# Kernel tuning notes

Hardware: AMD Instinct MI355X
Metric: run time of the kernel (lower is better)

## Reference

```python
import jax, jax.numpy as jnp
import numpy as np

N = 80000
E = 1280000
EPS = 1e-5

def _lrelu(x):
    return jax.nn.leaky_relu(x, 0.01)

def _bn(h):
    # training-mode BatchNorm1d with batch size 1: stats over the node dim; affine is identity at init
    return (h - h.mean(0)) / jnp.sqrt(h.var(0) + EPS)

def _ln(h, g, b):
    m = h.mean(-1, keepdims=True)
    v = h.var(-1, keepdims=True)
    return (h - m) / jnp.sqrt(v + EPS) * g + b

def _gcn(h, w, b, src, dst, n):
    # PyG GCNConv: add self loops, symmetric deg^-1/2 normalization, aggregate at target
    hw = h @ w.T
    loop = jnp.arange(n, dtype=src.dtype)
    s = jnp.concatenate([src, loop])
    d = jnp.concatenate([dst, loop])
    deg = jax.ops.segment_sum(jnp.ones(d.shape, hw.dtype), d, num_segments=n)
    dinv = jnp.where(deg > 0, 1.0 / jnp.sqrt(deg), 0.0)
    msg = hw[s] * (dinv[s] * dinv[d])[:, None]  # [E+N, C]
    return jax.ops.segment_sum(msg, d, num_segments=n) + b

def _tnet(x, c1w, c1b, c2w, c2b, c3w, c3b, f1w, f1b, f2w, f2b, f3w, f3b):
    h = jax.nn.relu(x @ c1w.T + c1b)          # [N,64]  (source skips bn1)
    h = jax.nn.relu(_bn(h @ c2w.T + c2b))     # [N,128]
    h = jax.nn.relu(_bn(h @ c3w.T + c3b))     # [N,1024]
    g = h.max(0)                              # global max pool -> [1024]
    g = jax.nn.relu(g @ f1w.T + f1b)
    g = jax.nn.relu(g @ f2w.T + f2b)
    iden = jnp.array([1.0, 0.0, 0.0, 0.0, 1.0, 0.0, 0.0, 0.0, 1.0], x.dtype)
    g = g @ f3w.T + f3b + iden
    return g.reshape(3, 3)

def _forward(edge_index, x, tnet_c1_w, tnet_c1_b, tnet_c2_w, tnet_c2_b, tnet_c3_w, tnet_c3_b, tnet_fc1_w, tnet_fc1_b, tnet_fc2_w, tnet_fc2_b, tnet_fc3_w, tnet_fc3_b, conv1_w, conv1_b, g1_li_w, g1_li_b, g1_gcn_w, g1_gcn_b, g1_ln_g, g1_ln_b, conv2_w, conv2_b, g2_li_w, g2_li_b, g2_gcn_w, g2_gcn_b, g2_ln_g, g2_ln_b, conv3_w, conv3_b, out_w, out_b):
    src, dst = edge_index[0], edge_index[1]
    n = x.shape[0]
    T = _tnet(x, tnet_c1_w, tnet_c1_b, tnet_c2_w, tnet_c2_b, tnet_c3_w, tnet_c3_b, tnet_fc1_w, tnet_fc1_b, tnet_fc2_w, tnet_fc2_b, tnet_fc3_w, tnet_fc3_b)
    h0 = x @ T                                  # [N,3] spatial transform
    xg = _lrelu(h0 @ conv1_w.T + conv1_b)       # [N,64] (conv1d k=1 == per-node linear)
    # Gcn_Attention 1
    nf = _lrelu(xg @ g1_li_w.T + g1_li_b)
    nf2 = _lrelu(_gcn(nf, g1_gcn_w, g1_gcn_b, src, dst, n))
    h = _ln(jnp.concatenate([nf, nf2], 1), g1_ln_g, g1_ln_b)   # [N,128]
    h = _lrelu(h @ conv2_w.T + conv2_b)
    # Gcn_Attention 2
    nf = _lrelu(h @ g2_li_w.T + g2_li_b)
    nf2 = _lrelu(_gcn(nf, g2_gcn_w, g2_gcn_b, src, dst, n))
    h = _ln(jnp.concatenate([nf, nf2], 1), g2_ln_g, g2_ln_b)   # [N,256]
    h = jnp.concatenate([h, xg], 1)                            # [N,320]
    h = _lrelu(h @ conv3_w.T + conv3_b)                        # [N,256]
    pooled = h.mean(0)                                         # global mean pool (single graph)
    feat = jnp.concatenate([jnp.broadcast_to(pooled, (n, pooled.shape[0])), xg], 1)  # [N,320]
    return feat @ out_w.T + out_b                              # [N,4]

def setup_inputs():
    ki = iter(jax.random.split(jax.random.key(0), 32))
    def W(shape):
        return jax.random.normal(next(ki), shape, jnp.float32) * (1.0 / float(np.sqrt(shape[-1])))
    z = lambda n: jnp.zeros((n,), jnp.float32)
    o = lambda n: jnp.ones((n,), jnp.float32)
    inp = {}
    inp['x'] = jax.random.normal(next(ki), (N, 3), jnp.float32)
    inp['edge_index'] = jax.random.randint(next(ki), (2, E), 0, N, dtype=jnp.int32)
    inp['tnet_c1_w'] = W((64, 3)); inp['tnet_c1_b'] = z(64)
    inp['tnet_c2_w'] = W((128, 64)); inp['tnet_c2_b'] = z(128)
    inp['tnet_c3_w'] = W((1024, 128)); inp['tnet_c3_b'] = z(1024)
    inp['tnet_fc1_w'] = W((512, 1024)); inp['tnet_fc1_b'] = z(512)
    inp['tnet_fc2_w'] = W((256, 512)); inp['tnet_fc2_b'] = z(256)
    inp['tnet_fc3_w'] = W((9, 256)); inp['tnet_fc3_b'] = z(9)
    inp['conv1_w'] = W((64, 3)); inp['conv1_b'] = z(64)
    inp['g1_li_w'] = W((64, 64)); inp['g1_li_b'] = z(64)
    inp['g1_gcn_w'] = W((64, 64)); inp['g1_gcn_b'] = z(64)
    inp['g1_ln_g'] = o(128); inp['g1_ln_b'] = z(128)
    inp['conv2_w'] = W((128, 128)); inp['conv2_b'] = z(128)
    inp['g2_li_w'] = W((128, 128)); inp['g2_li_b'] = z(128)
    inp['g2_gcn_w'] = W((128, 128)); inp['g2_gcn_b'] = z(128)
    inp['g2_ln_g'] = o(256); inp['g2_ln_b'] = z(256)
    inp['conv3_w'] = W((256, 320)); inp['conv3_b'] = z(256)
    inp['out_w'] = W((4, 320)); inp['out_b'] = z(4)
    return inp

def reference(x, edge_index, tnet_c1_w, tnet_c1_b, tnet_c2_w, tnet_c2_b, tnet_c3_w, tnet_c3_b, tnet_fc1_w, tnet_fc1_b, tnet_fc2_w, tnet_fc2_b, tnet_fc3_w, tnet_fc3_b, conv1_w, conv1_b, g1_li_w, g1_li_b, g1_gcn_w, g1_gcn_b, g1_ln_g, g1_ln_b, conv2_w, conv2_b, g2_li_w, g2_li_b, g2_gcn_w, g2_gcn_b, g2_ln_g, g2_ln_b, conv3_w, conv3_b, out_w, out_b):
    return _forward(edge_index, x, tnet_c1_w, tnet_c1_b, tnet_c2_w, tnet_c2_b, tnet_c3_w, tnet_c3_b, tnet_fc1_w, tnet_fc1_b, tnet_fc2_w, tnet_fc2_b, tnet_fc3_w, tnet_fc3_b, conv1_w, conv1_b, g1_li_w, g1_li_b, g1_gcn_w, g1_gcn_b, g1_ln_g, g1_ln_b, conv2_w, conv2_b, g2_li_w, g2_li_b, g2_gcn_w, g2_gcn_b, g2_ln_g, g2_ln_b, conv3_w, conv3_b, out_w, out_b)
```

## Files before the change

### kernel.cpp

```cpp
#include <hip/hip_runtime.h>
#include <cstddef>

#define EPSV 1e-5f

typedef __attribute__((ext_vector_type(8))) short frag8;
typedef __attribute__((ext_vector_type(4))) float f32x4;

__device__ __forceinline__ float lrelu01(float v) { return v > 0.f ? v : 0.01f * v; }
__device__ __forceinline__ void atomAddF(float* p, float v) { unsafeAtomicAdd(p, v); }
__device__ __forceinline__ unsigned fkey(float f) {
    unsigned u = __float_as_uint(f);
    return (u & 0x80000000u) ? ~u : (u | 0x80000000u);
}
__device__ __forceinline__ unsigned short f2b(float f) {
    unsigned u = __float_as_uint(f);
    unsigned r = u + 0x7fffu + ((u >> 16) & 1u);
    return (unsigned short)(r >> 16);
}
__device__ __forceinline__ float b2f(unsigned short h) {
    return __uint_as_float(((unsigned)h) << 16);
}
__device__ __forceinline__ float blo(unsigned u) { return __uint_as_float(u << 16); }
__device__ __forceinline__ float bhi(unsigned u) { return __uint_as_float(u & 0xffff0000u); }

static inline unsigned cdivu(unsigned a, unsigned b) { return (a + b - 1) / b; }


__global__ void k_degrank(const int* __restrict__ dst, int* __restrict__ deg,
                          int* __restrict__ rank, int E) {
    int e = blockIdx.x * 256 + threadIdx.x;
    if (e < E) rank[e] = atomicAdd(&deg[dst[e]], 1);
}

__global__ void k_scan_local(const int* __restrict__ deg, int* __restrict__ startv,
                             int* __restrict__ bsum, float* __restrict__ dinv, int n) {
    __shared__ int t0[256];
    int tid = threadIdx.x;
    int i = blockIdx.x * 256 + tid;
    int v = (i < n) ? deg[i] : 0;
    if (i < n) dinv[i] = rsqrtf((float)(v + 1));
    t0[tid] = v;
    __syncthreads();
    for (int o = 1; o < 256; o <<= 1) {
        int add = (tid >= o) ? t0[tid - o] : 0;
        __syncthreads();
        t0[tid] += add;
        __syncthreads();
    }
    if (i < n) startv[i] = t0[tid] - v;
    if (tid == 255) bsum[blockIdx.x] = t0[255];
}

__global__ void k_scan_bsum(int* __restrict__ bsum, int nb) {
    __shared__ int t0[512];
    int tid = threadIdx.x;
    int v = (tid < nb) ? bsum[tid] : 0;
    t0[tid] = v;
    __syncthreads();
    for (int o = 1; o < 512; o <<= 1) {
        int add = (tid >= o) ? t0[tid - o] : 0;
        __syncthreads();
        t0[tid] += add;
        __syncthreads();
    }
    if (tid < nb) bsum[tid] = t0[tid] - v;
}

__global__ void k_scan_add(int* __restrict__ startv, const int* __restrict__ bsum, int n) {
    int i = blockIdx.x * 256 + threadIdx.x;
    if (i < n) startv[i] += bsum[blockIdx.x];
}

__global__ void k_fill(const int* __restrict__ src, const int* __restrict__ dst,
                       const int* __restrict__ rank, const int* __restrict__ startv,
                       int* __restrict__ csr, int E) {
    int e = blockIdx.x * 256 + threadIdx.x;
    if (e < E) csr[startv[dst[e]] + rank[e]] = src[e];
}

template <int CH>
__launch_bounds__(256)
__global__ void k_gln(const int* __restrict__ startv, const int* __restrict__ degv,
                      const int* __restrict__ csr, const unsigned short* __restrict__ q,
                      const unsigned short* __restrict__ nf, const float* __restrict__ dinv,
                      const float* __restrict__ gcn_b, const float* __restrict__ lng,
                      const float* __restrict__ lnb, unsigned short* __restrict__ outp,
                      int ldo, int n) {
    const int wv = threadIdx.x >> 6, lane = threadIdx.x & 63;
    const int g = lane >> 4, p = lane & 15;
    int node = blockIdx.x * 4 + wv;
    if (node >= n) return;
    constexpr int CPL = CH / 16;
    constexpr int DPL = CPL / 2;

    float acc[CPL];
#pragma unroll
    for (int k = 0; k < CPL; ++k) acc[k] = 0.f;

    {
        unsigned su[DPL];
        const unsigned short* qrow = q + (size_t)node * CH + p * CPL;
        if (DPL == 4) *(uint4*)su = *(const uint4*)qrow;
        else          *(uint2*)su = *(const uint2*)qrow;
        if (g == 0) {
#pragma unroll
            for (int d = 0; d < DPL; ++d) { acc[2 * d] += blo(su[d]); acc[2 * d + 1] += bhi(su[d]); }
        }
    }

    int s0 = startv[node], cnt = degv[node];
    int sidx[4];
#pragma unroll
    for (int t = 0; t < 4; ++t) { int j = t * 4 + g; sidx[t] = (j < cnt) ? csr[s0 + j] : 0; }
    for (int j0 = 0; j0 < cnt; j0 += 16) {
        unsigned buf[4][DPL];
#pragma unroll
        for (int t = 0; t < 4; ++t) {
            const unsigned short* src = q + (size_t)sidx[t] * CH + p * CPL;
            if (DPL == 4) *(uint4*)buf[t] = *(const uint4*)src;
            else          *(uint2*)buf[t] = *(const uint2*)src;
        }
        int nsidx[4];
#pragma unroll
        for (int t = 0; t < 4; ++t) {
            int j = j0 + 16 + t * 4 + g;
            nsidx[t] = (j < cnt) ? csr[s0 + j] : 0;
        }
#pragma unroll
        for (int t = 0; t < 4; ++t) {
            if (j0 + t * 4 + g < cnt) {
#pragma unroll
                for (int d = 0; d < DPL; ++d) {
                    acc[2 * d] += blo(buf[t][d]);
                    acc[2 * d + 1] += bhi(buf[t][d]);
                }
            }
        }
#pragma unroll
        for (int t = 0; t < 4; ++t) sidx[t] = nsidx[t];
    }

#pragma unroll
    for (int k = 0; k < CPL; ++k) {
        acc[k] += __shfl_xor(acc[k], 16);
        acc[k] += __shfl_xor(acc[k], 32);
    }

    float di = dinv[node];
    float nv[CPL], bv[CPL];
    {
        unsigned su[DPL];
        const unsigned short* nrow = nf + (size_t)node * CH + p * CPL;
        if (DPL == 4) *(uint4*)su = *(const uint4*)nrow;
        else          *(uint2*)su = *(const uint2*)nrow;
#pragma unroll
        for (int d = 0; d < DPL; ++d) { nv[2 * d] = blo(su[d]); nv[2 * d + 1] = bhi(su[d]); }
    }
    const float* gb = gcn_b + p * CPL;
#pragma unroll
    for (int k = 0; k < CPL; ++k) bv[k] = lrelu01(di * acc[k] + gb[k]);

    float s = 0.f, ss = 0.f;
#pragma unroll
    for (int k = 0; k < CPL; ++k) { s += nv[k] + bv[k]; ss += nv[k] * nv[k] + bv[k] * bv[k]; }
#pragma unroll
    for (int off = 32; off > 0; off >>= 1) { s += __shfl_xor(s, off); ss += __shfl_xor(ss, off); }
    const float inv = 1.f / (float)(8 * CH);
    float mu = s * inv;
    float var = ss * inv - mu * mu;
    float rsg = rsqrtf(var + EPSV);

    unsigned short* orow = outp + (size_t)node * ldo;
    if (g == 0) {
        unsigned short tmp[CPL];
        const float* lg = lng + p * CPL; const float* lb = lnb + p * CPL;
#pragma unroll
        for (int k = 0; k < CPL; ++k) tmp[k] = f2b((nv[k] - mu) * rsg * lg[k] + lb[k]);
        if (DPL == 4) *(uint4*)(orow + p * CPL) = *(uint4*)tmp;
        else          *(uint2*)(orow + p * CPL) = *(uint2*)tmp;
    } else if (g == 1) {
        unsigned short tmp[CPL];
        const float* lg = lng + CH + p * CPL; const float* lb = lnb + CH + p * CPL;
#pragma unroll
        for (int k = 0; k < CPL; ++k) tmp[k] = f2b((bv[k] - mu) * rsg * lg[k] + lb[k]);
        if (DPL == 4) *(uint4*)(orow + CH + p * CPL) = *(uint4*)tmp;
        else          *(uint2*)(orow + CH + p * CPL) = *(uint2*)tmp;
    }
}


__global__ void k_wconv(const float* __restrict__ s0, const float* __restrict__ s1,
                        const float* __restrict__ s2, const float* __restrict__ s3,
                        const float* __restrict__ s4, const float* __restrict__ s5,
                        const float* __restrict__ s6, const float* __restrict__ s7,
                        unsigned short* __restrict__ dst) {
    int t = blockIdx.x * 256 + threadIdx.x;
    if (t >= 278528) return;
    const float* srcs[8] = {s0, s1, s2, s3, s4, s5, s6, s7};
    const int off[9] = {0, 8192, 139264, 143360, 147456, 163840, 180224, 196608, 278528};
    int seg = 0;
    while (t >= off[seg + 1]) ++seg;
    unsigned short v = f2b(srcs[seg][t - off[seg]]);
    if (seg == 1) {
        int li = t - 8192;
        int rch = li >> 7, k = li & 127;
        int cb = rch >> 7, r = rch & 127;
        int flat = ((r >> 4) * 4 + (k >> 5)) * 64 + ((k >> 3) & 3) * 16 + (r & 15);
        dst[8192 + cb * 16384 + flat * 8 + (k & 7)] = v;
    } else {
        dst[t] = v;
    }
}

__global__ void k_h1(const float* __restrict__ x, const float* __restrict__ w,
                     const float* __restrict__ b, unsigned short* __restrict__ h1, int n) {
    int node = blockIdx.x * 256 + threadIdx.x;
    if (node >= n) return;
    float x0 = x[node * 3], x1 = x[node * 3 + 1], x2 = x[node * 3 + 2];
    unsigned short* o = h1 + (size_t)node * 64;
#pragma unroll
    for (int cp = 0; cp < 8; ++cp) {
        unsigned short tmp[8];
#pragma unroll
        for (int t = 0; t < 8; ++t) {
            int c = cp * 8 + t;
            float v = x0 * w[c * 3] + x1 * w[c * 3 + 1] + x2 * w[c * 3 + 2] + b[c];
            tmp[t] = f2b(fmaxf(v, 0.f));
        }
        *(float4*)(o + cp * 8) = *(float4*)tmp;
    }
}

__global__ void k_prebn(const float* __restrict__ z, const float* __restrict__ sum2,
                        const float* __restrict__ ss2, unsigned short* __restrict__ a3f,
                        int n16, float invn) {
    int t = blockIdx.x * 256 + threadIdx.x;
    if (t >= n16) return;
    int row = t >> 4, cp = t & 15;
    int c = cp * 8;
    const float* src = z + (size_t)row * 128 + c;
    float4 v0 = *(const float4*)src;
    float4 v1 = *(const float4*)(src + 4);
    float vv[8] = {v0.x, v0.y, v0.z, v0.w, v1.x, v1.y, v1.z, v1.w};
    unsigned short o[8];
#pragma unroll
    for (int i = 0; i < 8; ++i) {
        float m = sum2[c + i] * invn;
        float var = ss2[c + i] * invn - m * m;
        o[i] = f2b(fmaxf((vv[i] - m) * rsqrtf(var + EPSV), 0.f));
    }
    int tile = row >> 7, r = row & 127;
    int flat = ((r >> 4) * 4 + (cp >> 2)) * 64 + (cp & 3) * 16 + (r & 15);
    *(float4*)(a3f + (size_t)tile * 16384 + flat * 8) = *(float4*)o;
}

__launch_bounds__(256)
__global__ void k_fc1(const float* __restrict__ sum3, const float* __restrict__ ss3,
                      const unsigned* __restrict__ maxk,
                      const float* __restrict__ f1w, const float* __restrict__ f1b,
                      float* __restrict__ a1, float invn) {
    __shared__ float g[1024];
    int tid = threadIdx.x;
    for (int c = tid; c < 1024; c += 256) {
        float m = sum3[c] * invn;
        float var = ss3[c] * invn - m * m;
        unsigned k = maxk[c];
        unsigned u = (k & 0x80000000u) ? (k & 0x7FFFFFFFu) : ~k;
        g[c] = fmaxf((__uint_as_float(u) - m) * rsqrtf(var + EPSV), 0.f);
    }
    __syncthreads();
    int row = blockIdx.x * 64 + (tid >> 2);
    int part = tid & 3;
    const float* w = f1w + (size_t)row * 1024 + part * 256;
    const float* gg = g + part * 256;
    float s = 0.f;
    for (int k = 0; k < 256; ++k) s = fmaf(w[k], gg[k], s);
    s += __shfl_xor(s, 1); s += __shfl_xor(s, 2);
    if (part == 0) a1[row] = fmaxf(s + f1b[row], 0.f);
}

__launch_bounds__(256)
__global__ void k_fc23(const float* __restrict__ a1, const float* __restrict__ f2w,
                       const float* __restrict__ f2b, const float* __restrict__ f3w,
                       const float* __restrict__ f3b, float* __restrict__ T9) {
    __shared__ float a2[256];
    int tid = threadIdx.x;
    {
        const float* w = f2w + (size_t)tid * 512;
        float s = f2b[tid];
        for (int k = 0; k < 512; ++k) s = fmaf(w[k], a1[k], s);
        a2[tid] = fmaxf(s, 0.f);
    }
    __syncthreads();
    if (tid < 9) {
        const float* w = f3w + (size_t)tid * 256;
        float s = f3b[tid];
        for (int k = 0; k < 256; ++k) s = fmaf(w[k], a2[k], s);
        if (tid == 0 || tid == 4 || tid == 8) s += 1.f;
        T9[tid] = s;
    }
}

__global__ void k_xg(const float* __restrict__ x, const float* __restrict__ T9,
                     const float* __restrict__ w, const float* __restrict__ b,
                     unsigned short* __restrict__ xg, int n) {
    int node = blockIdx.x * 256 + threadIdx.x;
    if (node >= n) return;
    float x0 = x[node * 3], x1 = x[node * 3 + 1], x2 = x[node * 3 + 2];
    float h0 = x0 * T9[0] + x1 * T9[3] + x2 * T9[6];
    float h1 = x0 * T9[1] + x1 * T9[4] + x2 * T9[7];
    float h2 = x0 * T9[2] + x1 * T9[5] + x2 * T9[8];
    unsigned short* o = xg + (size_t)node * 320;
#pragma unroll
    for (int cp = 0; cp < 8; ++cp) {
        unsigned short tmp[8];
#pragma unroll
        for (int t = 0; t < 8; ++t) {
            int c = cp * 8 + t;
            float v = h0 * w[c * 3] + h1 * w[c * 3 + 1] + h2 * w[c * 3 + 2] + b[c];
            tmp[t] = f2b(lrelu01(v));
        }
        *(float4*)(o + cp * 8) = *(float4*)tmp;
    }
}

__global__ void k_const4(const float* __restrict__ pooled, const float* __restrict__ ow,
                         const float* __restrict__ ob, float* __restrict__ c4, float invn) {
    int j = threadIdx.x >> 6, lane = threadIdx.x & 63;
    float s = 0.f;
    for (int c = lane; c < 256; c += 64) s += pooled[c] * invn * ow[j * 320 + c];
#pragma unroll
    for (int off = 32; off > 0; off >>= 1) s += __shfl_down(s, off);
    if (lane == 0) c4[j] = s + ob[j];
}

__global__ void k_out(const unsigned short* __restrict__ hcat, const float* __restrict__ ow,
                      const float* __restrict__ c4, float* __restrict__ out, int n) {
    int node = blockIdx.x * 256 + threadIdx.x;
    if (node >= n) return;
    const unsigned short* xgp = hcat + (size_t)node * 320 + 256;
    float s0 = c4[0], s1 = c4[1], s2 = c4[2], s3 = c4[3];
#pragma unroll
    for (int cp = 0; cp < 8; ++cp) {
        float4 raw = *(const float4*)(xgp + cp * 8);
        unsigned short tmp[8];
        *(float4*)tmp = raw;
#pragma unroll
        for (int t = 0; t < 8; ++t) {
            int k = 256 + cp * 8 + t;
            float f = b2f(tmp[t]);
            s0 = fmaf(f, ow[k], s0);
            s1 = fmaf(f, ow[320 + k], s1);
            s2 = fmaf(f, ow[640 + k], s2);
            s3 = fmaf(f, ow[960 + k], s3);
        }
    }
    *(float4*)(out + (size_t)node * 4) = make_float4(s0, s1, s2, s3);
}

enum { MF_BIAS = 1, MF_LRELU = 2, MF_DINV = 4, MF_STOREF = 8, MF_STOREB = 16,
       MF_STATS = 32, MF_COLSUM = 64 };

template <int BN, int MODE>
__launch_bounds__(256)
__global__ void k_mgemm(const unsigned short* __restrict__ A, int lda, int K,
                        const unsigned short* __restrict__ W,
                        const float* __restrict__ bias,
                        float* __restrict__ OutF, unsigned short* __restrict__ OutB, int ldo,
                        const float* __restrict__ dinv,
                        float* __restrict__ sum_o, float* __restrict__ ss_o,
                        unsigned* __restrict__ maxk_o) {
    constexpr int BM = 128;
    constexpr int LDT = 40;
    __shared__ unsigned short As[BM * LDT];
    __shared__ unsigned short Ws[BN * LDT];
    __shared__ float redS[2 * 128];
    __shared__ unsigned redM[128];

    const int tid = threadIdx.x;
    const int wid = tid >> 6, lane = tid & 63;
    const int quad = lane >> 4, lrow = lane & 15;
    const int bn0 = blockIdx.x * BM;
    const int bc0 = blockIdx.y * BN;

    constexpr int NI = (BN == 128) ? 4 : 2;
    constexpr int NJ = 4;
    const int wm = (BN == 128) ? (wid & 1) * 64 : wid * 32;
    const int wn = (BN == 128) ? (wid >> 1) * 64 : 0;

    if (MODE & (MF_STATS | MF_COLSUM)) {
        for (int c = tid; c < BN; c += 256) {
            redS[c] = 0.f; redS[128 + c] = 0.f; redM[c] = 0u;
        }
    }

    f32x4 acc[NI][NJ] = {};

    for (int k0 = 0; k0 < K; k0 += 32) {
#pragma unroll
        for (int h = 0; h < 2; ++h) {
            int ch = tid + h * 256;
            int row = ch >> 2, cp = ch & 3;
            const unsigned short* src = A + (size_t)(bn0 + row) * lda + k0 + cp * 8;
            *(float4*)&As[row * LDT + cp * 8] = *(const float4*)src;
        }
#pragma unroll
        for (int h = 0; h < BN / 64; ++h) {
            int ch = tid + h * 256;
            int row = ch >> 2, cp = ch & 3;
            const unsigned short* src = W + (size_t)(bc0 + row) * K + k0 + cp * 8;
            *(float4*)&Ws[row * LDT + cp * 8] = *(const float4*)src;
        }
        __syncthreads();
        frag8 af[NI], bf[NJ];
#pragma unroll
        for (int i = 0; i < NI; ++i)
            af[i] = *(const frag8*)&As[(wm + i * 16 + lrow) * LDT + quad * 8];
#pragma unroll
        for (int j = 0; j < NJ; ++j)
            bf[j] = *(const frag8*)&Ws[(wn + j * 16 + lrow) * LDT + quad * 8];
#pragma unroll
        for (int i = 0; i < NI; ++i)
#pragma unroll
            for (int j = 0; j < NJ; ++j)
                acc[i][j] = __builtin_amdgcn_mfma_f32_16x16x32_bf16(af[i], bf[j], acc[i][j], 0, 0, 0);
        __syncthreads();
    }

#pragma unroll
    for (int j = 0; j < NJ; ++j) {
        const int col = bc0 + wn + j * 16 + lrow;
        float bv = (MODE & MF_BIAS) ? bias[col] : 0.f;
        float s = 0.f, q = 0.f, m = -3.4e38f;
#pragma unroll
        for (int i = 0; i < NI; ++i) {
            const int rowb = bn0 + wm + i * 16 + quad * 4;
#pragma unroll
            for (int r = 0; r < 4; ++r) {
                float t = acc[i][j][r] + bv;
                if (MODE & MF_LRELU) t = lrelu01(t);
                if (MODE & MF_DINV) t *= dinv[rowb + r];
                if (MODE & MF_STOREF) OutF[(size_t)(rowb + r) * ldo + col] = t;
                if (MODE & MF_STOREB) OutB[(size_t)(rowb + r) * ldo + col] = f2b(t);
                s += t; q += t * t; m = fmaxf(m, t);
            }
        }
        if (MODE & (MF_STATS | MF_COLSUM)) {
            s += __shfl_xor(s, 16); s += __shfl_xor(s, 32);
            if (MODE & MF_STATS) {
                q += __shfl_xor(q, 16); q += __shfl_xor(q, 32);
                m = fmaxf(m, __shfl_xor(m, 16)); m = fmaxf(m, __shfl_xor(m, 32));
            }
            if (quad == 0) {
                int lc = wn + j * 16 + lrow;
                atomicAdd(&redS[lc], s);
                if (MODE & MF_STATS) {
                    atomicAdd(&redS[128 + lc], q);
                    atomicMax(&redM[lc], fkey(m));
                }
            }
        }
    }
    if (MODE & (MF_STATS | MF_COLSUM)) {
        __syncthreads();
        for (int c = tid; c < BN; c += 256) {
            atomAddF(&sum_o[bc0 + c], redS[c]);
            if (MODE & MF_STATS) {
                atomAddF(&ss_o[bc0 + c], redS[128 + c]);
                atomicMax(&maxk_o[bc0 + c], redM[c]);
            }
        }
    }
}

template <int BN>
__launch_bounds__(256)
__global__ void k_ligc(const unsigned short* __restrict__ A, int lda, int K,
                       const unsigned short* __restrict__ Wli, const float* __restrict__ bli,
                       const unsigned short* __restrict__ Wgc, const float* __restrict__ dinv,
                       unsigned short* __restrict__ NF, int ldnf,
                       unsigned short* __restrict__ Q, int ldq) {
    constexpr int BM = 128;
    constexpr int LDT = 40;
    constexpr int LDT2 = BN + 8;
    __shared__ unsigned short SA[BM * LDT2];
    __shared__ unsigned short Ws[BN * LDT];

    const int tid = threadIdx.x;
    const int wid = tid >> 6, lane = tid & 63;
    const int quad = lane >> 4, lrow = lane & 15;
    const int bn0 = blockIdx.x * BM;
    constexpr int NI = (BN == 128) ? 4 : 2;
    constexpr int NJ = 4;
    const int wm = (BN == 128) ? (wid & 1) * 64 : wid * 32;
    const int wn = (BN == 128) ? (wid >> 1) * 64 : 0;

    {
        f32x4 acc[NI][NJ] = {};
        for (int k0 = 0; k0 < K; k0 += 32) {
#pragma unroll
            for (int h = 0; h < 2; ++h) {
                int ch = tid + h * 256;
                int row = ch >> 2, cp = ch & 3;
                *(float4*)&SA[row * LDT + cp * 8] =
                    *(const float4*)(A + (size_t)(bn0 + row) * lda + k0 + cp * 8);
            }
#pragma unroll
            for (int h = 0; h < BN / 64; ++h) {
                int ch = tid + h * 256;
                int row = ch >> 2, cp = ch & 3;
                *(float4*)&Ws[row * LDT + cp * 8] =
                    *(const float4*)(Wli + (size_t)row * K + k0 + cp * 8);
            }
            __syncthreads();
            frag8 af[NI], bf[NJ];
#pragma unroll
            for (int i = 0; i < NI; ++i)
                af[i] = *(const frag8*)&SA[(wm + i * 16 + lrow) * LDT + quad * 8];
#pragma unroll
            for (int j = 0; j < NJ; ++j)
                bf[j] = *(const frag8*)&Ws[(wn + j * 16 + lrow) * LDT + quad * 8];
#pragma unroll
            for (int i = 0; i < NI; ++i)
#pragma unroll
                for (int j = 0; j < NJ; ++j)
                    acc[i][j] = __builtin_amdgcn_mfma_f32_16x16x32_bf16(af[i], bf[j], acc[i][j], 0, 0, 0);
            __syncthreads();
        }
#pragma unroll
        for (int j = 0; j < NJ; ++j) {
            const int col = wn + j * 16 + lrow;
            float bv = bli[col];
#pragma unroll
            for (int i = 0; i < NI; ++i) {
                const int rowl = wm + i * 16 + quad * 4;
#pragma unroll
                for (int r = 0; r < 4; ++r) {
                    unsigned short h = f2b(lrelu01(acc[i][j][r] + bv));
                    NF[(size_t)(bn0 + rowl + r) * ldnf + col] = h;
                    SA[(rowl + r) * LDT2 + col] = h;
                }
            }
        }
        __syncthreads();
    }
    {
        f32x4 acc[NI][NJ] = {};
        for (int k0 = 0; k0 < BN; k0 += 32) {
#pragma unroll
            for (int h = 0; h < BN / 64; ++h) {
                int ch = tid + h * 256;
                int row = ch >> 2, cp = ch & 3;
                *(float4*)&Ws[row * LDT + cp * 8] =
                    *(const float4*)(Wgc + (size_t)row * BN + k0 + cp * 8);
            }
            __syncthreads();
            frag8 af[NI], bf[NJ];
#pragma unroll
            for (int i = 0; i < NI; ++i)
                af[i] = *(const frag8*)&SA[(wm + i * 16 + lrow) * LDT2 + k0 + quad * 8];
#pragma unroll
            for (int j = 0; j < NJ; ++j)
                bf[j] = *(const frag8*)&Ws[(wn + j * 16 + lrow) * LDT + quad * 8];
#pragma unroll
            for (int i = 0; i < NI; ++i)
#pragma unroll
                for (int j = 0; j < NJ; ++j)
                    acc[i][j] = __builtin_amdgcn_mfma_f32_16x16x32_bf16(af[i], bf[j], acc[i][j], 0, 0, 0);
            __syncthreads();
        }
#pragma unroll
        for (int j = 0; j < NJ; ++j) {
            const int col = wn + j * 16 + lrow;
#pragma unroll
            for (int i = 0; i < NI; ++i) {
                const int rowb = bn0 + wm + i * 16 + quad * 4;
#pragma unroll
                for (int r = 0; r < 4; ++r) {
                    float t = acc[i][j][r] * dinv[rowb + r];
                    Q[(size_t)(rowb + r) * ldq + col] = f2b(t);
                }
            }
        }
    }
}

__launch_bounds__(256)
__global__ void k_z3(const unsigned short* __restrict__ AF,
                     const unsigned short* __restrict__ WF,
                     const float* __restrict__ bias,
                     float* __restrict__ sum_o, float* __restrict__ ss_o,
                     unsigned* __restrict__ maxk_o, int ntiles) {
    const int tid = threadIdx.x;
    const int wid = tid >> 6, lane = tid & 63;
    const int quad = lane >> 4, lrow = lane & 15;

    int bid = blockIdx.x;
    int w = (bid & 7) * ntiles + (bid >> 3);
    const int tile = w >> 3;
    const int cb = w & 7;
    const unsigned short* At = AF + (size_t)tile * 16384;
    const unsigned short* Wt = WF + (size_t)cb * 16384;

    const int ar = (wid & 1) * 4;
    const int wc = (wid >> 1) * 4;
    f32x4 acc[4][4] = {};
#pragma unroll
    for (int kc = 0; kc < 4; ++kc) {
        frag8 af[4], bf[4];
#pragma unroll
        for (int i = 0; i < 4; ++i)
            af[i] = *(const frag8*)&At[(((ar + i) * 4 + kc) * 64 + lane) * 8];
#pragma unroll
        for (int j = 0; j < 4; ++j)
            bf[j] = *(const frag8*)&Wt[(((wc + j) * 4 + kc) * 64 + lane) * 8];
#pragma unroll
        for (int i = 0; i < 4; ++i)
#pragma unroll
            for (int j = 0; j < 4; ++j)
                acc[i][j] = __builtin_amdgcn_mfma_f32_16x16x32_bf16(af[i], bf[j], acc[i][j], 0, 0, 0);
    }

#pragma unroll
    for (int j = 0; j < 4; ++j) {
        int c = cb * 128 + (wc + j) * 16 + lrow;
        float bv = bias[c];
        float s = 0.f, q = 0.f, m = -3.4e38f;
#pragma unroll
        for (int i = 0; i < 4; ++i)
#pragma unroll
            for (int r = 0; r < 4; ++r) {
                float t = acc[i][j][r] + bv;
                s += t; q += t * t; m = fmaxf(m, t);
            }
        s += __shfl_xor(s, 16); s += __shfl_xor(s, 32);
        q += __shfl_xor(q, 16); q += __shfl_xor(q, 32);
        m = fmaxf(m, __shfl_xor(m, 16)); m = fmaxf(m, __shfl_xor(m, 32));
        if (quad == 0) {
            atomAddF(&sum_o[c], s);
            atomAddF(&ss_o[c], q);
            atomicMax(&maxk_o[c], fkey(m));
        }
    }
}


extern "C" void kernel_launch(void* const* d_in, const int* in_sizes, int n_in,
                              void* d_out, int out_size, void* d_ws, size_t ws_size,
                              hipStream_t stream) {
    const float* x   = (const float*)d_in[0];
    const int*   ei  = (const int*)d_in[1];
    const float* c1w = (const float*)d_in[2];  const float* c1b = (const float*)d_in[3];
    const float* c2w = (const float*)d_in[4];  const float* c2b = (const float*)d_in[5];
    const float* c3w = (const float*)d_in[6];  const float* c3b = (const float*)d_in[7];
    const float* f1w = (const float*)d_in[8];  const float* f1b = (const float*)d_in[9];
    const float* f2w = (const float*)d_in[10]; const float* f2b = (const float*)d_in[11];
    const float* f3w = (const float*)d_in[12]; const float* f3b = (const float*)d_in[13];
    const float* cv1w = (const float*)d_in[14]; const float* cv1b = (const float*)d_in[15];
    const float* li1w = (const float*)d_in[16]; const float* li1b = (const float*)d_in[17];
    const float* gc1w = (const float*)d_in[18]; const float* gc1b = (const float*)d_in[19];
    const float* ln1g = (const float*)d_in[20]; const float* ln1b = (const float*)d_in[21];
    const float* cv2w = (const float*)d_in[22]; const float* cv2b = (const float*)d_in[23];
    const float* li2w = (const float*)d_in[24]; const float* li2b = (const float*)d_in[25];
    const float* gc2w = (const float*)d_in[26]; const float* gc2b = (const float*)d_in[27];
    const float* ln2g = (const float*)d_in[28]; const float* ln2b = (const float*)d_in[29];
    const float* cv3w = (const float*)d_in[30]; const float* cv3b = (const float*)d_in[31];
    const float* ow  = (const float*)d_in[32]; const float* ob  = (const float*)d_in[33];
    float* out = (float*)d_out;

    const int N = in_sizes[0] / 3;
    const int E = in_sizes[1] / 2;
    const int* srcI = ei;
    const int* dstI = ei + E;

    char* base = (char*)d_ws;
    size_t off = 0;
    auto take = [&](size_t bytes) -> char* {
        char* p = base + off;
        off = (off + bytes + 255) & ~(size_t)255;
        return p;
    };
    int*   deg    = (int*)  take((size_t)N * 4);
    float* dinv   = (float*)take((size_t)N * 4);
    int*   startv = (int*)  take((size_t)N * 4);
    int*   rank   = (int*)  take((size_t)E * 4);
    int*   csr    = (int*)  take((size_t)E * 4);
    int*   bsum   = (int*)  take(512 * 4);
    float* sm     = (float*)take(8192 * 4);
    unsigned short* WB = (unsigned short*)take(278528 * 2);
    unsigned short* H  = (unsigned short*)take((size_t)N * 320 * 2);
    float* F1 = (float*)take((size_t)N * 128 * 4);
    unsigned short* B1 = (unsigned short*)take((size_t)N * 64 * 2);
    unsigned short* B2 = (unsigned short*)take((size_t)N * 128 * 2);
    unsigned short* B3 = (unsigned short*)take((size_t)N * 128 * 2);

    unsigned short* c2wb  = WB + 0;
    unsigned short* c3wf  = WB + 8192;
    unsigned short* li1wb = WB + 139264;
    unsigned short* gc1wb = WB + 143360;
    unsigned short* cv2wb = WB + 147456;
    unsigned short* li2wb = WB + 163840;
    unsigned short* gc2wb = WB + 180224;
    unsigned short* cv3wb = WB + 196608;

    float* sum2 = sm + 0;    float* ss2 = sm + 128;
    float* sum3 = sm + 256;  float* ss3 = sm + 1280;
    unsigned* maxk = (unsigned*)(sm + 2304);
    float* pooled = sm + 3328;
    unsigned* dmax = (unsigned*)(sm + 3584);
    float* T9  = sm + 3968; float* c4 = sm + 3984;
    float* a1  = sm + 5120;

    const float invn = 1.0f / (float)N;
    const dim3 blk(256);
    const unsigned GX = (unsigned)(N / 128);
    const unsigned NB = cdivu((unsigned)N, 256);

    hipMemsetAsync(deg, 0, (size_t)N * 4, stream);
    hipMemsetAsync(sm, 0, 3712 * 4, stream);

    k_degrank<<<cdivu(E, 256), blk, 0, stream>>>(dstI, deg, rank, E);
    k_scan_local<<<NB, blk, 0, stream>>>(deg, startv, bsum, dinv, N);
    k_scan_bsum<<<1, 512, 0, stream>>>(bsum, (int)NB);
    k_scan_add<<<NB, blk, 0, stream>>>(startv, bsum, N);
    k_fill<<<cdivu(E, 256), blk, 0, stream>>>(srcI, dstI, rank, startv, csr, E);

    k_wconv<<<cdivu(278528, 256), blk, 0, stream>>>(c2w, c3w, li1w, gc1w, cv2w, li2w, gc2w, cv3w, WB);

    k_h1<<<cdivu((unsigned)N, 256), blk, 0, stream>>>(x, c1w, c1b, B1, N);
    k_mgemm<128, (MF_BIAS | MF_STOREF | MF_STATS)><<<dim3(GX, 1), blk, 0, stream>>>(
        B1, 64, 64, c2wb, c2b, F1, nullptr, 128, nullptr, sum2, ss2, dmax);
    k_prebn<<<cdivu((unsigned)N * 16, 256), blk, 0, stream>>>(F1, sum2, ss2, B2, N * 16, invn);
    k_z3<<<8 * GX, blk, 0, stream>>>(B2, c3wf, c3b, sum3, ss3, maxk, (int)GX);
    k_fc1<<<8, blk, 0, stream>>>(sum3, ss3, maxk, f1w, f1b, a1, invn);
    k_fc23<<<1, blk, 0, stream>>>(a1, f2w, f2b, f3w, f3b, T9);
    k_xg<<<cdivu((unsigned)N, 256), blk, 0, stream>>>(x, T9, cv1w, cv1b, H + 256, N);

    k_ligc<64><<<GX, blk, 0, stream>>>(H + 256, 320, 64, li1wb, li1b, gc1wb, dinv, B1, 64, B2, 64);
    k_gln<64><<<cdivu((unsigned)N, 4), blk, 0, stream>>>(
        startv, deg, csr, B2, B1, dinv, gc1b, ln1g, ln1b, B3, 128, N);
    k_mgemm<128, (MF_BIAS | MF_LRELU | MF_STOREB)><<<dim3(GX, 1), blk, 0, stream>>>(
        B3, 128, 128, cv2wb, cv2b, nullptr, B2, 128, nullptr, nullptr, nullptr, nullptr);

    k_ligc<128><<<GX, blk, 0, stream>>>(B2, 128, 128, li2wb, li2b, gc2wb, dinv, B3, 128, B2, 128);
    k_gln<128><<<cdivu((unsigned)N, 4), blk, 0, stream>>>(
        startv, deg, csr, B2, B3, dinv, gc2b, ln2g, ln2b, H, 320, N);

    k_mgemm<128, (MF_BIAS | MF_LRELU | MF_COLSUM)><<<dim3(GX, 2), blk, 0, stream>>>(
        H, 320, 320, cv3wb, cv3b, nullptr, nullptr, 0, nullptr, pooled, nullptr, nullptr);

    k_const4<<<1, 256, 0, stream>>>(pooled, ow, ob, c4, invn);
    k_out<<<cdivu((unsigned)N, 256), blk, 0, stream>>>(H, ow, c4, out, N);
}
```

Measured before the change: 544.2 us.

## Partition CSR build into destination passes and pad gather with zero row

Replaces the rank-based CSR construction with multi-pass degree counting and cursor-based filling, where each of 8 grid-y passes only handles destinations in one span. This drops the per-edge rank array and tries to improve atomic locality. The GCN gather loop now points out-of-range slots at a zero-filled padding row, so the per-slot bounds check goes away, and it accumulates in packed float2. In exchange, every pass re-reads the full edge list (8x the dst reads). Fill order within a node is now nondeterministic, which can change float summation order.

```diff
diff --git a/kernel.cpp b/kernel.cpp
--- a/kernel.cpp
+++ b/kernel.cpp
@@ -5,6 +5,7 @@
 
 typedef __attribute__((ext_vector_type(8))) short frag8;
 typedef __attribute__((ext_vector_type(4))) float f32x4;
+typedef __attribute__((ext_vector_type(2))) float f32x2;
 
 __device__ __forceinline__ float lrelu01(float v) { return v > 0.f ? v : 0.01f * v; }
 __device__ __forceinline__ void atomAddF(float* p, float v) { unsafeAtomicAdd(p, v); }
@@ -26,10 +27,12 @@
 static inline unsigned cdivu(unsigned a, unsigned b) { return (a + b - 1) / b; }
 
 
-__global__ void k_degrank(const int* __restrict__ dst, int* __restrict__ deg,
-                          int* __restrict__ rank, int E) {
+__global__ void k_degp(const int* __restrict__ dst, int* __restrict__ deg, int E, int span) {
     int e = blockIdx.x * 256 + threadIdx.x;
-    if (e < E) rank[e] = atomicAdd(&deg[dst[e]], 1);
+    if (e >= E) return;
+    int d = dst[e];
+    int lo = blockIdx.y * span;
+    if (d >= lo && d < lo + span) atomicAdd(&deg[d], 1);
 }
 
 __global__ void k_scan_local(const int* __restrict__ deg, int* __restrict__ startv,
@@ -66,16 +69,26 @@
     if (tid < nb) bsum[tid] = t0[tid] - v;
 }
 
-__global__ void k_scan_add(int* __restrict__ startv, const int* __restrict__ bsum, int n) {
+__global__ void k_scan_add(int* __restrict__ startv, const int* __restrict__ bsum,
+                           int* __restrict__ cursor, int n) {
     int i = blockIdx.x * 256 + threadIdx.x;
-    if (i < n) startv[i] += bsum[blockIdx.x];
-}
-
-__global__ void k_fill(const int* __restrict__ src, const int* __restrict__ dst,
-                       const int* __restrict__ rank, const int* __restrict__ startv,
-                       int* __restrict__ csr, int E) {
+    if (i < n) {
+        int s = startv[i] + bsum[blockIdx.x];
+        startv[i] = s;
+        cursor[i] = s;
+    }
+}
+
+__global__ void k_fillp(const int* __restrict__ src, const int* __restrict__ dst,
+                        int* __restrict__ cursor, int* __restrict__ csr, int E, int span) {
     int e = blockIdx.x * 256 + threadIdx.x;
-    if (e < E) csr[startv[dst[e]] + rank[e]] = src[e];
+    if (e >= E) return;
+    int d = dst[e];
+    int lo = blockIdx.y * span;
+    if (d >= lo && d < lo + span) {
+        int pos = atomicAdd(&cursor[d], 1);
+        csr[pos] = src[e];
+    }
 }
 
 template <int CH>
@@ -93,9 +106,9 @@
     constexpr int CPL = CH / 16;
     constexpr int DPL = CPL / 2;
 
-    float acc[CPL];
-#pragma unroll
-    for (int k = 0; k < CPL; ++k) acc[k] = 0.f;
+    f32x2 acc2[DPL];
+#pragma unroll
+    for (int d = 0; d < DPL; ++d) acc2[d] = (f32x2){0.f, 0.f};
 
     {
         unsigned su[DPL];
@@ -104,14 +117,14 @@
         else          *(uint2*)su = *(const uint2*)qrow;
         if (g == 0) {
 #pragma unroll
-            for (int d = 0; d < DPL; ++d) { acc[2 * d] += blo(su[d]); acc[2 * d + 1] += bhi(su[d]); }
+            for (int d = 0; d < DPL; ++d) acc2[d] += (f32x2){blo(su[d]), bhi(su[d])};
         }
     }
 
     int s0 = startv[node], cnt = degv[node];
     int sidx[4];
 #pragma unroll
-    for (int t = 0; t < 4; ++t) { int j = t * 4 + g; sidx[t] = (j < cnt) ? csr[s0 + j] : 0; }
+    for (int t = 0; t < 4; ++t) { int j = t * 4 + g; sidx[t] = (j < cnt) ? csr[s0 + j] : n; }
     for (int j0 = 0; j0 < cnt; j0 += 16) {
         unsigned buf[4][DPL];
 #pragma unroll
@@ -120,26 +133,21 @@
             if (DPL == 4) *(uint4*)buf[t] = *(const uint4*)src;
             else          *(uint2*)buf[t] = *(const uint2*)src;
         }
-        int nsidx[4];
 #pragma unroll
         for (int t = 0; t < 4; ++t) {
             int j = j0 + 16 + t * 4 + g;
-            nsidx[t] = (j < cnt) ? csr[s0 + j] : 0;
-        }
-#pragma unroll
-        for (int t = 0; t < 4; ++t) {
-            if (j0 + t * 4 + g < cnt) {
-#pragma unroll
-                for (int d = 0; d < DPL; ++d) {
-                    acc[2 * d] += blo(buf[t][d]);
-                    acc[2 * d + 1] += bhi(buf[t][d]);
-                }
-            }
-        }
-#pragma unroll
-        for (int t = 0; t < 4; ++t) sidx[t] = nsidx[t];
-    }
-
+            sidx[t] = (j < cnt) ? csr[s0 + j] : n;
+        }
+#pragma unroll
+        for (int t = 0; t < 4; ++t)
+#pragma unroll
+            for (int d = 0; d < DPL; ++d)
+                acc2[d] += (f32x2){blo(buf[t][d]), bhi(buf[t][d])};
+    }
+
+    float acc[CPL];
+#pragma unroll
+    for (int d = 0; d < DPL; ++d) { acc[2 * d] = acc2[d].x; acc[2 * d + 1] = acc2[d].y; }
 #pragma unroll
     for (int k = 0; k < CPL; ++k) {
         acc[k] += __shfl_xor(acc[k], 16);
@@ -683,7 +691,7 @@
     int*   deg    = (int*)  take((size_t)N * 4);
     float* dinv   = (float*)take((size_t)N * 4);
     int*   startv = (int*)  take((size_t)N * 4);
-    int*   rank   = (int*)  take((size_t)E * 4);
+    int*   cursor = (int*)  take((size_t)N * 4);
     int*   csr    = (int*)  take((size_t)E * 4);
     int*   bsum   = (int*)  take(512 * 4);
     float* sm     = (float*)take(8192 * 4);
@@ -691,7 +699,7 @@
     unsigned short* H  = (unsigned short*)take((size_t)N * 320 * 2);
     float* F1 = (float*)take((size_t)N * 128 * 4);
     unsigned short* B1 = (unsigned short*)take((size_t)N * 64 * 2);
-    unsigned short* B2 = (unsigned short*)take((size_t)N * 128 * 2);
+    unsigned short* B2 = (unsigned short*)take(((size_t)N + 1) * 128 * 2);
     unsigned short* B3 = (unsigned short*)take((size_t)N * 128 * 2);
 
     unsigned short* c2wb  = WB + 0;
@@ -715,15 +723,19 @@
     const dim3 blk(256);
     const unsigned GX = (unsigned)(N / 128);
     const unsigned NB = cdivu((unsigned)N, 256);
+    const int PASS = 8;
+    const int span = (int)cdivu((unsigned)N, PASS);
+    const dim3 egrid(cdivu(E, 256), PASS);
 
     hipMemsetAsync(deg, 0, (size_t)N * 4, stream);
     hipMemsetAsync(sm, 0, 3712 * 4, stream);
-
-    k_degrank<<<cdivu(E, 256), blk, 0, stream>>>(dstI, deg, rank, E);
+    hipMemsetAsync(B2 + (size_t)N * 128, 0, 256, stream);
+
+    k_degp<<<egrid, blk, 0, stream>>>(dstI, deg, E, span);
     k_scan_local<<<NB, blk, 0, stream>>>(deg, startv, bsum, dinv, N);
     k_scan_bsum<<<1, 512, 0, stream>>>(bsum, (int)NB);
-    k_scan_add<<<NB, blk, 0, stream>>>(startv, bsum, N);
-    k_fill<<<cdivu(E, 256), blk, 0, stream>>>(srcI, dstI, rank, startv, csr, E);
+    k_scan_add<<<NB, blk, 0, stream>>>(startv, bsum, cursor, N);
+    k_fillp<<<egrid, blk, 0, stream>>>(srcI, dstI, cursor, csr, E, span);
 
     k_wconv<<<cdivu(278528, 256), blk, 0, stream>>>(c2w, c3w, li1w, gc1w, cv2w, li2w, gc2w, cv3w, WB);
 
@@ -732,6 +744,7 @@
         B1, 64, 64, c2wb, c2b, F1, nullptr, 128, nullptr, sum2, ss2, dmax);
     k_prebn<<<cdivu((unsigned)N * 16, 256), blk, 0, stream>>>(F1, sum2, ss2, B2, N * 16, invn);
     k_z3<<<8 * GX, blk, 0, stream>>>(B2, c3wf, c3b, sum3, ss3, maxk, (int)GX);
+    hipMemsetAsync(B2 + (size_t)N * 64, 0, 128, stream);
     k_fc1<<<8, blk, 0, stream>>>(sum3, ss3, maxk, f1w, f1b, a1, invn);
     k_fc23<<<1, blk, 0, stream>>>(a1, f2w, f2b, f3w, f3b, T9);
     k_xg<<<cdivu((unsigned)N, 256), blk, 0, stream>>>(x, T9, cv1w, cv1b, H + 256, N);
```

Result: slower. 617.1 us (+13.4%).
